# Kernel optimization log

Measured on AMD Instinct MI355X. Metric: run time of the kernel, lower is better.

Reference implementation:

```python
import jax, jax.numpy as jnp
import numpy as np

NUM_HEADS = 12


def _build_mask(N, unseen_size, dtype):
    # Columns for the last `unseen_size` tokens are masked (-inf) for every
    # query row EXCEPT the diagonal entries in that block (each unseen token
    # may attend to itself). Matches the original Python-loop construction.
    idx = jnp.arange(N)
    col_unseen = idx[None, :] >= (N - unseen_size)
    off_diag = idx[:, None] != idx[None, :]
    return jnp.where(col_unseen & off_diag, -jnp.inf, jnp.asarray(0.0, dtype))


def reference(x, w_qkv, w_proj, b_proj, unseen_size):
    B, N, C = x.shape
    H = NUM_HEADS
    d = C // H
    scale = d ** -0.5
    # qkv: (B,N,3C) -> (3,B,H,N,d)
    qkv = (x @ w_qkv.T).reshape(B, N, 3, H, d).transpose(2, 0, 3, 1, 4)
    q, k, v = qkv[0], qkv[1], qkv[2]
    attn = jnp.einsum('bhqd,bhkd->bhqk', q, k) * scale
    attn = attn + _build_mask(N, unseen_size, attn.dtype)  # broadcast (N,N)
    attn = jax.nn.softmax(attn, axis=-1)
    out = jnp.einsum('bhqk,bhkd->bhqd', attn, v)
    out = out.transpose(0, 2, 1, 3).reshape(B, N, C)
    return out @ w_proj.T + b_proj


def setup_inputs() -> dict:
    key = jax.random.key(0)
    k1, k2, k3 = jax.random.split(key, 3)
    B, N, C = 2, 2048, 768
    x = jax.random.normal(k1, (B, N, C), dtype=jnp.float32)
    w_qkv = jax.random.normal(k2, (3 * C, C), dtype=jnp.float32) * (C ** -0.5)
    w_proj = jax.random.normal(k3, (C, C), dtype=jnp.float32) * (C ** -0.5)
    b_proj = jnp.zeros((C,), dtype=jnp.float32)
    return {"x": x, "w_qkv": w_qkv, "w_proj": w_proj, "b_proj": b_proj,
            "unseen_size": 512}
```

## Files before the change

### kernel.cpp

```cpp
#include <hip/hip_runtime.h>
#include <math.h>

#define NH 12
#define DH 64
#define NSEQ 2048
#define NB 2
#define CDIM 768
#define NVIS 1536

typedef _Float16 half8 __attribute__((ext_vector_type(8)));
typedef _Float16 half4 __attribute__((ext_vector_type(4)));
typedef float floatx4 __attribute__((ext_vector_type(4)));

static constexpr size_t SZ_X    = (size_t)NB*NSEQ*CDIM;
static constexpr size_t SZ_WQKV = (size_t)3*CDIM*CDIM;
static constexpr size_t SZ_WP   = (size_t)CDIM*CDIM;
static constexpr size_t SZ_HEAD = (size_t)NB*NH*NSEQ*DH;

#define GLOAD_LDS16(gp, lp) \
  __builtin_amdgcn_global_load_lds((const __attribute__((address_space(1))) void*)(gp), \
                                   (__attribute__((address_space(3))) void*)(lp), 16, 0, 0)

__global__ __launch_bounds__(256) void convert_kernel(
    const float* __restrict__ x, const float* __restrict__ wqkv, const float* __restrict__ wp,
    _Float16* __restrict__ xb, _Float16* __restrict__ wqkvb, _Float16* __restrict__ wpb)
{
  size_t idx = ((size_t)blockIdx.x*256 + threadIdx.x)*4;
  const float* src; _Float16* dst; size_t off;
  if (idx < SZ_X)                        { src = x;    dst = xb;    off = idx; }
  else if (idx < SZ_X+SZ_WQKV)           { src = wqkv; dst = wqkvb; off = idx - SZ_X; }
  else if (idx < SZ_X+SZ_WQKV+SZ_WP)     { src = wp;   dst = wpb;   off = idx - SZ_X - SZ_WQKV; }
  else return;
  float4 v = *reinterpret_cast<const float4*>(src + off);
  _Float16 o[4] = {(_Float16)v.x,(_Float16)v.y,(_Float16)v.z,(_Float16)v.w};
  *reinterpret_cast<uint2*>(dst + off) = *reinterpret_cast<uint2*>(o);
}

template<int MODE, int BN>
__global__ __launch_bounds__(256) void gemm_bt(
    const _Float16* __restrict__ A, const _Float16* __restrict__ Bt,
    const float* __restrict__ bias,
    _Float16* __restrict__ qb, _Float16* __restrict__ kb, _Float16* __restrict__ vb,
    float* __restrict__ outp)
{
  constexpr int K = CDIM;
  constexpr int BM = 128, BK = 32;
  constexpr int MI = (BN == 128) ? 4 : 2;
  constexpr int NI = 4;
  __shared__ _Float16 As[BM*BK];
  __shared__ _Float16 Bs[BN*BK];
  const int tid = threadIdx.x;
  const int lane = tid & 63, wid = tid >> 6;
  const int l15 = lane & 15, quad = lane >> 4;
  const int wm = (BN == 128) ? (wid >> 1)*64 : wid*32;
  const int wn = (BN == 128) ? (wid & 1)*64 : 0;
  const int tileN = blockIdx.x*BN, tileM = blockIdx.y*BM;
  const int lrow = lane >> 2, lchunk = lane & 3;
  const int gcol = ((lchunk ^ (lrow >> 1)) & 3)*8;
  const _Float16* gA0 = A  + (size_t)(tileM + wid*32      + lrow)*K + gcol;
  const _Float16* gA1 = A  + (size_t)(tileM + wid*32 + 16 + lrow)*K + gcol;
  const _Float16* gB0 = Bt + (size_t)(tileN + ((BN==128) ? wid*32 : wid*16) + lrow)*K + gcol;
  const _Float16* gB1 = Bt + (size_t)(tileN + wid*32 + 16 + lrow)*K + gcol;
  _Float16* lA0 = As + (wid*32)*BK;
  _Float16* lA1 = As + (wid*32 + 16)*BK;
  _Float16* lB0 = Bs + ((BN==128) ? wid*32 : wid*16)*BK;
  _Float16* lB1 = Bs + (wid*32 + 16)*BK;
  const int cp = ((quad ^ (l15 >> 1)) & 3)*8;
  floatx4 acc[MI][NI] = {};
  for (int k0 = 0; k0 < K; k0 += BK) {
    __syncthreads();
    GLOAD_LDS16(gA0 + k0, lA0);
    GLOAD_LDS16(gA1 + k0, lA1);
    GLOAD_LDS16(gB0 + k0, lB0);
    if (BN == 128) GLOAD_LDS16(gB1 + k0, lB1);
    __syncthreads();
    half8 af[MI], bfr[NI];
    #pragma unroll
    for (int mi = 0; mi < MI; mi++)
      af[mi] = *reinterpret_cast<const half8*>(&As[(wm + mi*16 + l15)*BK + cp]);
    #pragma unroll
    for (int ni = 0; ni < NI; ni++)
      bfr[ni] = *reinterpret_cast<const half8*>(&Bs[(wn + ni*16 + l15)*BK + cp]);
    #pragma unroll
    for (int mi = 0; mi < MI; mi++)
      #pragma unroll
      for (int ni = 0; ni < NI; ni++)
        acc[mi][ni] = __builtin_amdgcn_mfma_f32_16x16x32_f16(af[mi], bfr[ni], acc[mi][ni], 0,0,0);
  }
  #pragma unroll
  for (int mi = 0; mi < MI; mi++)
    #pragma unroll
    for (int ni = 0; ni < NI; ni++) {
      int n = tileN + wn + ni*16 + l15;
      int m0 = tileM + wm + mi*16 + quad*4;
      if (MODE == 0) {
        int part = n / CDIM, rem = n - part*CDIM;
        int h = rem >> 6, dd = rem & 63;
        int b = m0 >> 11, i0 = m0 & 2047;
        if (part == 2) {
          half4 pk = {(_Float16)acc[mi][ni][0], (_Float16)acc[mi][ni][1],
                      (_Float16)acc[mi][ni][2], (_Float16)acc[mi][ni][3]};
          *reinterpret_cast<half4*>(&vb[(((size_t)b*NH + h)*DH + dd)*NSEQ + i0]) = pk;
        } else {
          _Float16* dst = part ? kb : qb;
          float sc = part ? 1.0f : 0.125f*1.44269504f;
          #pragma unroll
          for (int r = 0; r < 4; r++)
            dst[(((size_t)b*NH + h)*NSEQ + i0 + r)*DH + dd] = (_Float16)(acc[mi][ni][r]*sc);
        }
      } else {
        #pragma unroll
        for (int r = 0; r < 4; r++)
          outp[(size_t)(m0 + r)*CDIM + n] = acc[mi][ni][r] + bias[n];
      }
    }
}

__global__ __launch_bounds__(256, 3) void fa_kernel(
    const _Float16* __restrict__ qg, const _Float16* __restrict__ kg,
    const _Float16* __restrict__ vtg, _Float16* __restrict__ og)
{
  __shared__ _Float16 Ps[2][64*64];
  __shared__ float Ls[4*64];
  const int blk = blockIdx.x;
  const int idx = blk >> 3;
  const int bh = (blk & 7)*3 + (idx % 3);
  const int qbase = (idx / 3) * 64;
  const int tid = threadIdx.x;
  const int lane = tid & 63, w = tid >> 6;
  const int l15 = lane & 15, quad = lane >> 4;
  const int sw = (l15 & 7) << 3;
  const _Float16* qp  = qg  + (size_t)bh*NSEQ*DH;
  const _Float16* kbp = kg  + (size_t)bh*NSEQ*DH;
  const _Float16* vbp = vtg + (size_t)bh*DH*NSEQ;
  half8 qf[4][2];
  #pragma unroll
  for (int g = 0; g < 4; g++)
    #pragma unroll
    for (int c = 0; c < 2; c++)
      qf[g][c] = *reinterpret_cast<const half8*>(qp + (size_t)(qbase + g*16 + l15)*DH + c*32 + quad*8);
  const _Float16* kRow = kbp + (size_t)(w*16 + l15)*DH + quad*8;
  const _Float16* vRow = vbp + (size_t)(w*16 + l15)*NSEQ + quad*8;
  floatx4 o[4] = {};
  float lsum[4] = {0.f, 0.f, 0.f, 0.f};
  const int pws  = (w*16 + quad*4) ^ sw;
  const int prd0 = (quad*8) ^ sw;
  const int prd1 = (32 + quad*8) ^ sw;

  half8 kcur0 = *reinterpret_cast<const half8*>(kRow);
  half8 kcur1 = *reinterpret_cast<const half8*>(kRow + 32);
  {
    floatx4 st[4] = {};
    #pragma unroll
    for (int g = 0; g < 4; g++) {
      st[g] = __builtin_amdgcn_mfma_f32_16x16x32_f16(kcur0, qf[g][0], st[g], 0,0,0);
      st[g] = __builtin_amdgcn_mfma_f32_16x16x32_f16(kcur1, qf[g][1], st[g], 0,0,0);
    }
    #pragma unroll
    for (int g = 0; g < 4; g++) {
      float e0 = __builtin_exp2f(st[g][0]), e1 = __builtin_exp2f(st[g][1]);
      float e2 = __builtin_exp2f(st[g][2]), e3 = __builtin_exp2f(st[g][3]);
      lsum[g] += (e0+e1)+(e2+e3);
      half4 pk = {(_Float16)e0,(_Float16)e1,(_Float16)e2,(_Float16)e3};
      *reinterpret_cast<half4*>(&Ps[0][(g*16+l15)*64 + pws]) = pk;
    }
  }
  half8 vcur0 = *reinterpret_cast<const half8*>(vRow);
  half8 vcur1 = *reinterpret_cast<const half8*>(vRow + 32);
  kcur0 = *reinterpret_cast<const half8*>(kRow + (size_t)64*DH);
  kcur1 = *reinterpret_cast<const half8*>(kRow + (size_t)64*DH + 32);

  for (int t = 0; t < 23; t++) {
    floatx4 st[4] = {};
    __builtin_amdgcn_s_setprio(1);
    #pragma unroll
    for (int g = 0; g < 4; g++) {
      st[g] = __builtin_amdgcn_mfma_f32_16x16x32_f16(kcur0, qf[g][0], st[g], 0,0,0);
      st[g] = __builtin_amdgcn_mfma_f32_16x16x32_f16(kcur1, qf[g][1], st[g], 0,0,0);
    }
    __builtin_amdgcn_s_setprio(0);
    half4 pk[4];
    #pragma unroll
    for (int g = 0; g < 4; g++) {
      float e0 = __builtin_exp2f(st[g][0]), e1 = __builtin_exp2f(st[g][1]);
      float e2 = __builtin_exp2f(st[g][2]), e3 = __builtin_exp2f(st[g][3]);
      lsum[g] += (e0+e1)+(e2+e3);
      pk[g] = half4{(_Float16)e0,(_Float16)e1,(_Float16)e2,(_Float16)e3};
    }
    __syncthreads();
    const int tk = (t + 2 < 24) ? t + 2 : 0;
    half8 kn0 = *reinterpret_cast<const half8*>(kRow + (size_t)tk*64*DH);
    half8 kn1 = *reinterpret_cast<const half8*>(kRow + (size_t)tk*64*DH + 32);
    half8 vn0 = *reinterpret_cast<const half8*>(vRow + (t+1)*64);
    half8 vn1 = *reinterpret_cast<const half8*>(vRow + (t+1)*64 + 32);
    #pragma unroll
    for (int g = 0; g < 4; g++)
      *reinterpret_cast<half4*>(&Ps[(t+1)&1][(g*16+l15)*64 + pws]) = pk[g];
    __builtin_amdgcn_s_setprio(1);
    #pragma unroll
    for (int g = 0; g < 4; g++) {
      const _Float16* pb = &Ps[t&1][(g*16+l15)*64];
      half8 pb0 = *reinterpret_cast<const half8*>(pb + prd0);
      half8 pb1 = *reinterpret_cast<const half8*>(pb + prd1);
      o[g] = __builtin_amdgcn_mfma_f32_16x16x32_f16(vcur0, pb0, o[g], 0,0,0);
      o[g] = __builtin_amdgcn_mfma_f32_16x16x32_f16(vcur1, pb1, o[g], 0,0,0);
    }
    __builtin_amdgcn_s_setprio(0);
    kcur0 = kn0; kcur1 = kn1; vcur0 = vn0; vcur1 = vn1;
  }
  __syncthreads();
  #pragma unroll
  for (int g = 0; g < 4; g++) {
    const _Float16* pb = &Ps[1][(g*16+l15)*64];
    half8 pb0 = *reinterpret_cast<const half8*>(pb + prd0);
    half8 pb1 = *reinterpret_cast<const half8*>(pb + prd1);
    o[g] = __builtin_amdgcn_mfma_f32_16x16x32_f16(vcur0, pb0, o[g], 0,0,0);
    o[g] = __builtin_amdgcn_mfma_f32_16x16x32_f16(vcur1, pb1, o[g], 0,0,0);
  }
  #pragma unroll
  for (int g = 0; g < 4; g++) {
    lsum[g] += __shfl_xor(lsum[g], 16);
    lsum[g] += __shfl_xor(lsum[g], 32);
  }
  if (lane < 16) {
    #pragma unroll
    for (int g = 0; g < 4; g++) Ls[w*64 + g*16 + lane] = lsum[g];
  }
  __syncthreads();
  float den[4];
  #pragma unroll
  for (int g = 0; g < 4; g++)
    den[g] = Ls[g*16+l15] + Ls[64+g*16+l15] + Ls[128+g*16+l15] + Ls[192+g*16+l15];
  if (qbase >= NVIS) {
    #pragma unroll
    for (int g = 0; g < 4; g++) {
      half8 kd0 = *reinterpret_cast<const half8*>(kbp + (size_t)(qbase + g*16 + l15)*DH + quad*8);
      half8 kd1 = *reinterpret_cast<const half8*>(kbp + (size_t)(qbase + g*16 + l15)*DH + 32 + quad*8);
      float pd = 0.f;
      #pragma unroll
      for (int j = 0; j < 8; j++)
        pd += (float)qf[g][0][j]*(float)kd0[j] + (float)qf[g][1][j]*(float)kd1[j];
      pd += __shfl_xor(pd, 16);
      pd += __shfl_xor(pd, 32);
      float e = __builtin_exp2f(pd);
      den[g] += e;
      #pragma unroll
      for (int r = 0; r < 4; r++)
        o[g][r] += e * (float)vbp[(size_t)(w*16+quad*4+r)*NSEQ + qbase + g*16 + l15];
    }
  }
  const int b = bh / NH, h = bh - b*NH;
  #pragma unroll
  for (int g = 0; g < 4; g++) {
    float inv = 1.0f / den[g];
    half4 pk = {(_Float16)(o[g][0]*inv), (_Float16)(o[g][1]*inv),
                (_Float16)(o[g][2]*inv), (_Float16)(o[g][3]*inv)};
    size_t oaddr = ((size_t)b*NSEQ + qbase + g*16 + l15)*CDIM + h*DH + w*16 + quad*4;
    *reinterpret_cast<half4*>(&og[oaddr]) = pk;
  }
}

extern "C" void kernel_launch(void* const* d_in, const int* in_sizes, int n_in,
                              void* d_out, int out_size, void* d_ws, size_t ws_size,
                              hipStream_t stream) {
  (void)in_sizes; (void)n_in; (void)out_size; (void)ws_size;
  const float* x     = (const float*)d_in[0];
  const float* wqkv  = (const float*)d_in[1];
  const float* wproj = (const float*)d_in[2];
  const float* bproj = (const float*)d_in[3];

  _Float16* xb    = (_Float16*)d_ws;
  _Float16* wqkvb = xb + SZ_X;
  _Float16* wpb   = wqkvb + SZ_WQKV;
  _Float16* qb    = wpb + SZ_WP;
  _Float16* kb    = qb + SZ_HEAD;
  _Float16* vb    = kb + SZ_HEAD;
  _Float16* ob    = vb + SZ_HEAD;
  float* outp = (float*)d_out;

  size_t total = SZ_X + SZ_WQKV + SZ_WP;
  int cblocks = (int)((total/4 + 255)/256);
  convert_kernel<<<cblocks, 256, 0, stream>>>(x, wqkv, wproj, xb, wqkvb, wpb);
  gemm_bt<0,128><<<dim3(3*CDIM/128, NB*NSEQ/128), 256, 0, stream>>>(xb, wqkvb, nullptr, qb, kb, vb, nullptr);
  fa_kernel<<<NB*NH*(NSEQ/64), 256, 0, stream>>>(qb, kb, vb, ob);
  gemm_bt<1,64><<<dim3(CDIM/64, NB*NSEQ/128), 256, 0, stream>>>(ob, wpb, bproj, nullptr, nullptr, nullptr, outp);
}
```

Measured before the change: 161.2 us.

## Stage V-transpose epilogue through LDS and widen output-projection GEMM tile

```diff
diff --git a/kernel.cpp b/kernel.cpp
--- a/kernel.cpp
+++ b/kernel.cpp
@@ -47,8 +47,11 @@
   constexpr int BM = 128, BK = 32;
   constexpr int MI = (BN == 128) ? 4 : 2;
   constexpr int NI = 4;
-  __shared__ _Float16 As[BM*BK];
-  __shared__ _Float16 Bs[BN*BK];
+  constexpr int LDT = 132;
+  constexpr int SMEM = (MODE == 0) ? 128*LDT : (BM*BK + BN*BK);
+  __shared__ _Float16 smem[SMEM];
+  _Float16* As = smem;
+  _Float16* Bs = smem + BM*BK;
   const int tid = threadIdx.x;
   const int lane = tid & 63, wid = tid >> 6;
   const int l15 = lane & 15, quad = lane >> 4;
@@ -87,6 +90,32 @@
       for (int ni = 0; ni < NI; ni++)
         acc[mi][ni] = __builtin_amdgcn_mfma_f32_16x16x32_f16(af[mi], bfr[ni], acc[mi][ni], 0,0,0);
   }
+  if (MODE == 0 && tileN >= 2*CDIM) {
+    __syncthreads();
+    #pragma unroll
+    for (int mi = 0; mi < MI; mi++)
+      #pragma unroll
+      for (int ni = 0; ni < NI; ni++) {
+        int nl = wn + ni*16 + l15;
+        int ml = wm + mi*16 + quad*4;
+        half4 pk = {(_Float16)acc[mi][ni][0], (_Float16)acc[mi][ni][1],
+                    (_Float16)acc[mi][ni][2], (_Float16)acc[mi][ni][3]};
+        *reinterpret_cast<half4*>(&smem[nl*LDT + ml]) = pk;
+      }
+    __syncthreads();
+    const int b = tileM >> 11;
+    const int i0b = tileM & 2047;
+    #pragma unroll
+    for (int it = 0; it < 8; it++) {
+      int row = it*16 + (tid >> 4);
+      int chunk = tid & 15;
+      int rem = tileN + row - 2*CDIM;
+      int h = rem >> 6, dd = rem & 63;
+      half8 v8 = *reinterpret_cast<const half8*>(&smem[row*LDT + chunk*8]);
+      *reinterpret_cast<half8*>(&vb[(((size_t)b*NH + h)*DH + dd)*NSEQ + i0b + chunk*8]) = v8;
+    }
+    return;
+  }
   #pragma unroll
   for (int mi = 0; mi < MI; mi++)
     #pragma unroll
@@ -97,17 +126,11 @@
         int part = n / CDIM, rem = n - part*CDIM;
         int h = rem >> 6, dd = rem & 63;
         int b = m0 >> 11, i0 = m0 & 2047;
-        if (part == 2) {
-          half4 pk = {(_Float16)acc[mi][ni][0], (_Float16)acc[mi][ni][1],
-                      (_Float16)acc[mi][ni][2], (_Float16)acc[mi][ni][3]};
-          *reinterpret_cast<half4*>(&vb[(((size_t)b*NH + h)*DH + dd)*NSEQ + i0]) = pk;
-        } else {
-          _Float16* dst = part ? kb : qb;
-          float sc = part ? 1.0f : 0.125f*1.44269504f;
-          #pragma unroll
-          for (int r = 0; r < 4; r++)
-            dst[(((size_t)b*NH + h)*NSEQ + i0 + r)*DH + dd] = (_Float16)(acc[mi][ni][r]*sc);
-        }
+        _Float16* dst = part ? kb : qb;
+        float sc = part ? 1.0f : 0.125f*1.44269504f;
+        #pragma unroll
+        for (int r = 0; r < 4; r++)
+          dst[(((size_t)b*NH + h)*NSEQ + i0 + r)*DH + dd] = (_Float16)(acc[mi][ni][r]*sc);
       } else {
         #pragma unroll
         for (int r = 0; r < 4; r++)
@@ -283,5 +306,5 @@
   convert_kernel<<<cblocks, 256, 0, stream>>>(x, wqkv, wproj, xb, wqkvb, wpb);
   gemm_bt<0,128><<<dim3(3*CDIM/128, NB*NSEQ/128), 256, 0, stream>>>(xb, wqkvb, nullptr, qb, kb, vb, nullptr);
   fa_kernel<<<NB*NH*(NSEQ/64), 256, 0, stream>>>(qb, kb, vb, ob);
-  gemm_bt<1,64><<<dim3(CDIM/64, NB*NSEQ/128), 256, 0, stream>>>(ob, wpb, bproj, nullptr, nullptr, nullptr, outp);
+  gemm_bt<1,128><<<dim3(CDIM/128, NB*NSEQ/128), 256, 0, stream>>>(ob, wpb, bproj, nullptr, nullptr, nullptr, outp);
 }
```

New measurement: 159.3 us. Within noise of the previous version (-1.2%).
